# Kernel optimization log

Hardware: AMD Instinct MI355X
Metric: run time of the kernel (lower is better)

The kernel has to match this reference:

```python
import jax, jax.numpy as jnp
import numpy as np

N_NODES = 100000
N_EDGES = 1600000
IN_DIM = 128
EM_DIM = 64
HI_DIM = 64
OUT_DIM = 128
HEADS = 4


def setup_inputs() -> dict:
    key = jax.random.key(0)
    ks = jax.random.split(key, 16)
    s = 0.05  # small init scale to keep exp(a) well-conditioned
    return {
        "x_from": jax.random.normal(ks[0], (N_NODES, IN_DIM), jnp.float32),
        "edge_index": jax.random.randint(ks[1], (2, N_EDGES), 0, N_NODES, jnp.int32),
        "Wi1": jax.random.normal(ks[2], (HEADS, IN_DIM, EM_DIM), jnp.float32) * s,
        "bi1": jax.random.normal(ks[3], (HEADS, EM_DIM), jnp.float32) * s,
        "Wi2": jax.random.normal(ks[4], (HEADS, EM_DIM, EM_DIM), jnp.float32) * s,
        "bi2": jax.random.normal(ks[5], (HEADS, EM_DIM), jnp.float32) * s,
        "Wa1": jax.random.normal(ks[6], (HEADS, 2 * EM_DIM, HI_DIM), jnp.float32) * s,
        "ba1": jax.random.normal(ks[7], (HEADS, HI_DIM), jnp.float32) * s,
        "Wa2": jax.random.normal(ks[8], (HEADS, HI_DIM, 1), jnp.float32) * s,
        "ba2": jax.random.normal(ks[9], (HEADS, 1), jnp.float32) * s,
        "Wf1": jax.random.normal(ks[10], (HEADS * EM_DIM, HI_DIM), jnp.float32) * s,
        "bf1": jax.random.normal(ks[11], (HI_DIM,), jnp.float32) * s,
        "Wf2": jax.random.normal(ks[12], (HI_DIM, OUT_DIM), jnp.float32) * s,
        "bf2": jax.random.normal(ks[13], (OUT_DIM,), jnp.float32) * s,
    }


def reference(x_from, edge_index, Wi1, bi1, Wi2, bi2, Wa1, ba1, Wa2, ba2,
              Wf1, bf1, Wf2, bf2):
    n = x_from.shape[0]
    src, dst = edge_index[0], edge_index[1]

    # per-head node embedding MLP (layer_n=2, leaky_relu between layers)
    h1 = jax.nn.leaky_relu(jnp.einsum('nf,hfe->hne', x_from, Wi1) + bi1[:, None, :])
    hs = jnp.einsum('hne,hed->hnd', h1, Wi2) + bi2[:, None, :]  # [H, N, EM]
    # hs_to in the original is f_init(x_from) again -> identical to hs

    em = hs.shape[-1]
    # A(cat(h_src, h_dst)) first linear split per-node to avoid [H,E,2*EM] cat
    s_src = jnp.einsum('hne,hek->hnk', hs, Wa1[:, :em, :])  # [H, N, HI]
    s_dst = jnp.einsum('hne,hek->hnk', hs, Wa1[:, em:, :])  # [H, N, HI]
    t = jax.nn.leaky_relu(s_src[:, src] + s_dst[:, dst] + ba1[:, None, :])  # [H, E, HI]
    a = jax.nn.leaky_relu(jnp.einsum('hek,hko->heo', t, Wa2) + ba2[:, None, :])  # [H,E,1]

    e = jnp.exp(a)  # [H, E, 1]
    # softmax denominator is scatter_add over SRC (as in the source)
    e_sum = jax.vmap(lambda v: jax.ops.segment_sum(v, src, num_segments=n))(e)  # [H,N,1]
    alpha = e / e_sum[:, src]  # [H, E, 1]

    # attention-weighted aggregation: scatter_add of hs[src]*alpha onto dst
    msg = hs[:, src] * alpha  # [H, E, EM]
    agg = jax.vmap(lambda v: jax.ops.segment_sum(v, dst, num_segments=n))(msg)  # [H,N,EM]

    h_cat = jnp.transpose(agg, (1, 0, 2)).reshape(n, -1)  # [N, H*EM], head-major cat
    out = jax.nn.leaky_relu(h_cat @ Wf1 + bf1) @ Wf2 + bf2  # [N, OUT]
    return out
```

## Files before the change

kernel.cpp:

```cpp
#include <hip/hip_runtime.h>
#include <hip/hip_fp16.h>

#define NN 100000
#define NE 1600000
#define HEADS 4
#define EM 64
#define HF 256
#define IN_DIM 128
#define HI 64
#define OUT_DIM 128
#define NB_SCAN 391
#define SLOTS 56

using f16 = _Float16;
typedef _Float16 f16x2 __attribute__((ext_vector_type(2)));
typedef _Float16 f16x4 __attribute__((ext_vector_type(4)));
typedef float f32x2 __attribute__((ext_vector_type(2)));
typedef float f32x4 __attribute__((ext_vector_type(4)));
typedef int i32x4 __attribute__((ext_vector_type(4)));

__device__ __forceinline__ float lrelu(float x) { return fmaxf(x, 0.01f * x); }

__global__ __launch_bounds__(256) void k_wprep(
    const float* __restrict__ Wi1, const float* __restrict__ Wi2, const float* __restrict__ Wa1,
    uint2* __restrict__ Wi1f, uint2* __restrict__ Wi2f,
    uint2* __restrict__ Wsf, uint2* __restrict__ Wdf)
{
    int tid = blockIdx.x * 256 + threadIdx.x;
    int chunk = tid >> 6, lane = tid & 63;
    if (chunk >= 320) return;
    int g = lane >> 4, c = lane & 15;
    const float* wp;
    uint2* dst;
    if (chunk < 128) {
        int h = chunk >> 5, kc = (chunk >> 2) & 7, n = chunk & 3;
        wp = Wi1 + (size_t)h * IN_DIM * EM + (size_t)(kc * 16 + 4 * g) * EM + n * 16 + c;
        dst = Wi1f + chunk * 64 + lane;
    } else if (chunk < 192) {
        int idx = chunk - 128;
        int h = idx >> 4, kc = (idx >> 2) & 3, n = idx & 3;
        wp = Wi2 + (size_t)h * EM * EM + (size_t)(kc * 16 + 4 * g) * EM + n * 16 + c;
        dst = Wi2f + idx * 64 + lane;
    } else if (chunk < 256) {
        int idx = chunk - 192;
        int h = idx >> 4, kc = (idx >> 2) & 3, n = idx & 3;
        wp = Wa1 + (size_t)h * (2 * EM) * HI + (size_t)(kc * 16 + 4 * g) * HI + n * 16 + c;
        dst = Wsf + idx * 64 + lane;
    } else {
        int idx = chunk - 256;
        int h = idx >> 4, kc = (idx >> 2) & 3, n = idx & 3;
        wp = Wa1 + (size_t)h * (2 * EM) * HI + (size_t)(EM + kc * 16 + 4 * g) * HI + n * 16 + c;
        dst = Wdf + idx * 64 + lane;
    }
    f16x4 v = { (f16)wp[0], (f16)wp[EM], (f16)wp[2 * EM], (f16)wp[3 * EM] };
    *dst = __builtin_bit_cast(uint2, v);
}

__global__ __launch_bounds__(256) void k_embed(
    const float* __restrict__ x,
    const float* __restrict__ bi1, const float* __restrict__ bi2,
    const uint2* __restrict__ Wi1f, const uint2* __restrict__ Wi2f,
    const uint2* __restrict__ Wsf, const uint2* __restrict__ Wdf,
    const int* __restrict__ ei, int* __restrict__ cur_s, int* __restrict__ cur_d,
    int* __restrict__ es1,
    f16* __restrict__ hs, f16* __restrict__ ssrc, f16* __restrict__ sdst)
{
    __shared__ __align__(16) char smem[18432];
    f16 (*xh)[136]     = (f16(*)[136])smem;
    f16 (*hsL)[16][72] = (f16(*)[16][72])smem;
    f16 (*h1L)[16][72] = (f16(*)[16][72])(smem + 9216);

    const int t = threadIdx.x;
    const int base = blockIdx.x * 16;

    #pragma unroll
    for (int i = 0; i < 2; ++i) {
        int q = t + i * 256;
        int row = q >> 5;
        int c4 = (q & 31) << 2;
        float4 v = *(const float4*)(x + (size_t)(base + row) * IN_DIM + c4);
        f16x4 hv = { (f16)v.x, (f16)v.y, (f16)v.z, (f16)v.w };
        *(f16x4*)&xh[row][c4] = hv;
    }
    __syncthreads();

    const int h = t >> 6;
    const int l = t & 63;
    const int g = l >> 4;
    const int c = l & 15;

    const f32x4 z4 = { 0.f, 0.f, 0.f, 0.f };

    f32x4 acc1[4] = { z4, z4, z4, z4 };
    {
        const uint2* Wf = Wi1f + (size_t)h * 32 * 64;
        for (int kc = 0; kc < 8; ++kc) {
            f16x4 bf[4];
            #pragma unroll
            for (int n = 0; n < 4; ++n)
                bf[n] = __builtin_bit_cast(f16x4, Wf[(kc * 4 + n) * 64 + l]);
            f16x4 af = *(const f16x4*)&xh[c][kc * 16 + 4 * g];
            #pragma unroll
            for (int n = 0; n < 4; ++n)
                acc1[n] = __builtin_amdgcn_mfma_f32_16x16x16f16(af, bf[n], acc1[n], 0, 0, 0);
        }
    }
    __syncthreads();

    #pragma unroll
    for (int n = 0; n < 4; ++n) {
        float b = bi1[h * EM + n * 16 + c];
        #pragma unroll
        for (int r = 0; r < 4; ++r)
            h1L[h][4 * g + r][n * 16 + c] = (f16)lrelu(acc1[n][r] + b);
    }
    __syncthreads();

    f32x4 acc2[4] = { z4, z4, z4, z4 };
    {
        const uint2* Wf = Wi2f + (size_t)h * 16 * 64;
        for (int kc = 0; kc < 4; ++kc) {
            f16x4 bf[4];
            #pragma unroll
            for (int n = 0; n < 4; ++n)
                bf[n] = __builtin_bit_cast(f16x4, Wf[(kc * 4 + n) * 64 + l]);
            f16x4 af = *(const f16x4*)&h1L[h][c][kc * 16 + 4 * g];
            #pragma unroll
            for (int n = 0; n < 4; ++n)
                acc2[n] = __builtin_amdgcn_mfma_f32_16x16x16f16(af, bf[n], acc2[n], 0, 0, 0);
        }
    }
    #pragma unroll
    for (int n = 0; n < 4; ++n) {
        float b = bi2[h * EM + n * 16 + c];
        #pragma unroll
        for (int r = 0; r < 4; ++r)
            hsL[h][4 * g + r][n * 16 + c] = (f16)(acc2[n][r] + b);
    }
    __syncthreads();

    f16x4 af3[4];
    #pragma unroll
    for (int kc = 0; kc < 4; ++kc)
        af3[kc] = *(const f16x4*)&hsL[h][c][kc * 16 + 4 * g];

    {
        f32x4 acc3[4] = { z4, z4, z4, z4 };
        const uint2* Wf = Wsf + (size_t)h * 16 * 64;
        for (int kc = 0; kc < 4; ++kc) {
            f16x4 bf[4];
            #pragma unroll
            for (int n = 0; n < 4; ++n)
                bf[n] = __builtin_bit_cast(f16x4, Wf[(kc * 4 + n) * 64 + l]);
            #pragma unroll
            for (int n = 0; n < 4; ++n)
                acc3[n] = __builtin_amdgcn_mfma_f32_16x16x16f16(af3[kc], bf[n], acc3[n], 0, 0, 0);
        }
        #pragma unroll
        for (int n = 0; n < 4; ++n)
            #pragma unroll
            for (int r = 0; r < 4; ++r)
                h1L[h][4 * g + r][n * 16 + c] = (f16)acc3[n][r];
    }
    f32x4 acc3b[4] = { z4, z4, z4, z4 };
    {
        const uint2* Wf = Wdf + (size_t)h * 16 * 64;
        for (int kc = 0; kc < 4; ++kc) {
            f16x4 bf[4];
            #pragma unroll
            for (int n = 0; n < 4; ++n)
                bf[n] = __builtin_bit_cast(f16x4, Wf[(kc * 4 + n) * 64 + l]);
            #pragma unroll
            for (int n = 0; n < 4; ++n)
                acc3b[n] = __builtin_amdgcn_mfma_f32_16x16x16f16(af3[kc], bf[n], acc3b[n], 0, 0, 0);
        }
    }
    __syncthreads();

    #pragma unroll
    for (int i = 0; i < 2; ++i) {
        int q = t + i * 256;
        int hd = q >> 7, row = (q >> 3) & 15, c8 = (q & 7) << 3;
        int node = base + row;
        *(int4*)&hs[(size_t)node * HF + hd * EM + c8]   = *(int4*)&hsL[hd][row][c8];
        *(int4*)&ssrc[(size_t)node * HF + hd * EM + c8] = *(int4*)&h1L[hd][row][c8];
    }
    __syncthreads();

    #pragma unroll
    for (int n = 0; n < 4; ++n)
        #pragma unroll
        for (int r = 0; r < 4; ++r)
            hsL[h][4 * g + r][n * 16 + c] = (f16)acc3b[n][r];
    __syncthreads();
    #pragma unroll
    for (int i = 0; i < 2; ++i) {
        int q = t + i * 256;
        int hd = q >> 7, row = (q >> 3) & 15, c8 = (q & 7) << 3;
        int node = base + row;
        *(int4*)&sdst[(size_t)node * HF + hd * EM + c8] = *(int4*)&hsL[hd][row][c8];
    }

    {
        int e = blockIdx.x * 256 + t;
        int src = ei[e], dst = ei[NE + e];
        int pos_d = atomicAdd(cur_d + dst, 1);
        int pos_s = atomicAdd(cur_s + src, 1);
        if (pos_s < SLOTS) es1[src * SLOTS + pos_s] = (pos_d << 17) | dst;
    }
}

__global__ __launch_bounds__(256) void k_scan1(const int* __restrict__ arr, int* __restrict__ bsum)
{
    const int t = threadIdx.x, lane = t & 63, w = t >> 6;
    int i = blockIdx.x * 256 + t;
    int v = (i < NN) ? arr[i] : 0;
    #pragma unroll
    for (int d = 1; d < 64; d <<= 1) v += __shfl_xor(v, d);
    __shared__ int ws[4];
    if (lane == 0) ws[w] = v;
    __syncthreads();
    if (t == 0) bsum[blockIdx.x] = ws[0] + ws[1] + ws[2] + ws[3];
}

__global__ __launch_bounds__(256) void k_scan2(int* __restrict__ bsum)
{
    __shared__ int wsum[4], woff[4];
    __shared__ int base, ctot;
    const int t = threadIdx.x, lane = t & 63, w = t >> 6;
    if (t == 0) base = 0;
    __syncthreads();
    for (int start = 0; start < NB_SCAN; start += 256) {
        int i = start + t;
        int v = (i < NB_SCAN) ? bsum[i] : 0;
        int incl = v;
        #pragma unroll
        for (int d = 1; d < 64; d <<= 1) {
            int u = __shfl_up(incl, d);
            if (lane >= d) incl += u;
        }
        if (lane == 63) wsum[w] = incl;
        __syncthreads();
        if (t == 0) {
            int s = 0;
            #pragma unroll
            for (int j = 0; j < 4; ++j) { int xv = wsum[j]; woff[j] = s; s += xv; }
            ctot = s;
        }
        __syncthreads();
        if (i < NB_SCAN) bsum[i] = base + woff[w] + incl - v;
        __syncthreads();
        if (t == 0) base += ctot;
        __syncthreads();
    }
}

__global__ __launch_bounds__(256) void k_scan3(int* __restrict__ arr, const int* __restrict__ bsum)
{
    const int t = threadIdx.x, lane = t & 63, w = t >> 6;
    int i = blockIdx.x * 256 + t;
    int v = (i < NN) ? arr[i] : 0;
    int incl = v;
    #pragma unroll
    for (int d = 1; d < 64; d <<= 1) {
        int u = __shfl_up(incl, d);
        if (lane >= d) incl += u;
    }
    __shared__ int wsum[4], woff[4];
    if (lane == 63) wsum[w] = incl;
    __syncthreads();
    if (t == 0) {
        int s = 0;
        #pragma unroll
        for (int j = 0; j < 4; ++j) { int xv = wsum[j]; woff[j] = s; s += xv; }
    }
    __syncthreads();
    if (i < NN) arr[i] = bsum[blockIdx.x] + woff[w] + incl - v;
}

__global__ __launch_bounds__(256) void k_edge_att_csr(
    const int* __restrict__ es1, const int* __restrict__ cur_s,
    const f16* __restrict__ ssrc, const f16* __restrict__ sdst,
    const float* __restrict__ ba1, const float* __restrict__ Wa2, const float* __restrict__ ba2,
    const int* __restrict__ cur_d, i32x4* __restrict__ ed16, float* __restrict__ inv4)
{
    const int wave = threadIdx.x >> 6;
    const int lane = threadIdx.x & 63;
    const int n = blockIdx.x * 4 + wave;
    const int eidx = lane >> 4;
    const int q = lane & 15;
    const int h = q >> 2;
    const int fb = q * 16;

    int cnt = cur_s[n];
    if (cnt <= 0) return;
    if (cnt > SLOTS) cnt = SLOTS;

    int bslot = lane < cnt ? lane : cnt - 1;
    const int bval = es1[n * SLOTS + bslot];
    const int bdst = bval & 0x1FFFF;
    const int brec = cur_d[bdst] + (bval >> 17);

    f16x2 z[8], w[8];
    {
        const int4* sr = (const int4*)(ssrc + (size_t)n * HF + fb);
        int4 s0 = sr[0], s1 = sr[1];
        const f16x2* sp0 = (const f16x2*)&s0;
        const f16x2* sp1 = (const f16x2*)&s1;
        const float4* bb = (const float4*)(ba1 + fb);
        const float4* wwp = (const float4*)(Wa2 + fb);
        #pragma unroll
        for (int j = 0; j < 4; ++j) {
            float4 b4 = bb[j];
            float4 w4 = wwp[j];
            f16x2 blo = { (f16)b4.x, (f16)b4.y }, bhi = { (f16)b4.z, (f16)b4.w };
            f16x2 wlo = { (f16)w4.x, (f16)w4.y }, whi = { (f16)w4.z, (f16)w4.w };
            f16x2 sv = (j < 2) ? sp0[2 * j] : sp1[2 * (j - 2)];
            f16x2 sv2 = (j < 2) ? sp0[2 * j + 1] : sp1[2 * (j - 2) + 1];
            z[2 * j] = sv + blo;
            z[2 * j + 1] = sv2 + bhi;
            w[2 * j] = wlo;
            w[2 * j + 1] = whi;
        }
    }
    const float ba2v = ba2[h];
    const f16x2 c001 = { (f16)0.01f, (f16)0.01f };

    float esumv = 0.f;

    int r = 0;
    int slot0 = r + eidx; if (slot0 > cnt - 1) slot0 = cnt - 1;
    bool val = (r + eidx) < cnt;
    int dst_cur = __shfl(bdst, slot0);
    int rec_cur = __shfl(brec, slot0);
    const int4* dr = (const int4*)(sdst + (size_t)dst_cur * HF + fb);
    int4 d0 = dr[0], d1 = dr[1];

    while (r < cnt) {
        const int rn = r + 4;
        int4 nd0 = d0, nd1 = d1;
        int dst_nxt = dst_cur, rec_nxt = rec_cur;
        bool val_n = false;
        if (rn < cnt) {
            int slot = rn + eidx; if (slot > cnt - 1) slot = cnt - 1;
            val_n = (rn + eidx) < cnt;
            dst_nxt = __shfl(bdst, slot);
            rec_nxt = __shfl(brec, slot);
            const int4* dr2 = (const int4*)(sdst + (size_t)dst_nxt * HF + fb);
            nd0 = dr2[0]; nd1 = dr2[1];
        }

        const f16x2* dp0 = (const f16x2*)&d0;
        const f16x2* dp1 = (const f16x2*)&d1;
        float s = 0.f;
        #pragma unroll
        for (int j = 0; j < 4; ++j) {
            f16x2 u = z[j] + dp0[j];
            u = __builtin_elementwise_max(u, u * c001);
            s = __builtin_amdgcn_fdot2(u, w[j], s, false);
        }
        #pragma unroll
        for (int j = 0; j < 4; ++j) {
            f16x2 u = z[4 + j] + dp1[j];
            u = __builtin_elementwise_max(u, u * c001);
            s = __builtin_amdgcn_fdot2(u, w[4 + j], s, false);
        }
        s += __shfl_xor(s, 1);
        s += __shfl_xor(s, 2);
        float a = s + ba2v;
        a = fmaxf(a, 0.01f * a);
        float eh = val ? __expf(a) : 0.f;
        esumv += eh;

        {
            int b = lane & 48;
            float e1 = __shfl(eh, b + 4);
            float e2 = __shfl(eh, b + 8);
            float e3 = __shfl(eh, b + 12);
            if (val && q == 0) {
                f16x2 p01 = { (f16)eh, (f16)e1 };
                f16x2 p23 = { (f16)e2, (f16)e3 };
                i32x4 rec;
                rec.x = n;
                rec.y = 0;
                rec.z = (int)__builtin_bit_cast(uint, p01);
                rec.w = (int)__builtin_bit_cast(uint, p23);
                __builtin_nontemporal_store(rec, &ed16[rec_cur]);
            }
        }

        d0 = nd0; d1 = nd1; dst_cur = dst_nxt; rec_cur = rec_nxt; val = val_n;
        r = rn;
    }

    esumv += __shfl_xor(esumv, 16);
    esumv += __shfl_xor(esumv, 32);

    if (eidx == 0 && (q & 3) == 0)
        inv4[n * 4 + h] = 1.f / esumv;
}

__global__ __launch_bounds__(256) void k_aggregate_csr(
    const i32x4* __restrict__ ed16, const int* __restrict__ cur_d,
    const float* __restrict__ inv4,
    const f16* __restrict__ hs,
    f16* __restrict__ agg)
{
    const int wave = threadIdx.x >> 6;
    const int lane = threadIdx.x & 63;
    const int n = blockIdx.x * 4 + wave;
    const int eidx = lane >> 4;
    const int q = lane & 15;
    const int h = q >> 2;
    const int fb = q * 16;

    const int beg = cur_d[n];
    const int end = (n < NN - 1) ? cur_d[n + 1] : NE;

    const f32x2 z2 = { 0.f, 0.f };
    f32x2 acc[8];
    #pragma unroll
    for (int j = 0; j < 8; ++j) acc[j] = z2;

#define COMP_B(recV, ivV, hV0, hV1, valV)                                       \
    {                                                                           \
        uint sel = (h & 2) ? (uint)recV.w : (uint)recV.z;                       \
        f16x2 selh = __builtin_bit_cast(f16x2, sel);                            \
        float att = (float)((h & 1) ? selh.y : selh.x);                         \
        float al = valV ? att * ivV : 0.f;                                      \
        f32x2 al2 = { al, al };                                                 \
        const f16x2* hp0 = (const f16x2*)&hV0;                                  \
        const f16x2* hp1 = (const f16x2*)&hV1;                                  \
        _Pragma("unroll")                                                       \
        for (int j = 0; j < 4; ++j) {                                           \
            f16x2 f = hp0[j];                                                   \
            f32x2 fv = { (float)f.x, (float)f.y };                              \
            acc[j] += fv * al2;                                                 \
        }                                                                       \
        _Pragma("unroll")                                                       \
        for (int j = 0; j < 4; ++j) {                                           \
            f16x2 f = hp1[j];                                                   \
            f32x2 fv = { (float)f.x, (float)f.y };                              \
            acc[4 + j] += fv * al2;                                             \
        }                                                                       \
    }

    if (beg < end) {
        int p = beg;
        int idx0 = p + eidx; if (idx0 > end - 1) idx0 = end - 1;
        bool val = (p + eidx) < end;
        i32x4 rec = __builtin_nontemporal_load(&ed16[idx0]);
        float iv = inv4[rec.x * 4 + h];
        const int4* hr = (const int4*)(hs + (size_t)rec.x * HF + fb);
        int4 v0 = hr[0], v1 = hr[1];

        while (p < end) {
            const int pn = p + 4;
            i32x4 nrec = rec;
            float niv = iv;
            int4 nv0 = v0, nv1 = v1;
            bool val_n = false;
            if (pn < end) {
                int idx = pn + eidx; if (idx > end - 1) idx = end - 1;
                val_n = (pn + eidx) < end;
                nrec = __builtin_nontemporal_load(&ed16[idx]);
                niv = inv4[nrec.x * 4 + h];
                const int4* hr2 = (const int4*)(hs + (size_t)nrec.x * HF + fb);
                nv0 = hr2[0]; nv1 = hr2[1];
            }

            COMP_B(rec, iv, v0, v1, val);

            rec = nrec; iv = niv; v0 = nv0; v1 = nv1; val = val_n;
            p = pn;
        }
    }
#undef COMP_B

    #pragma unroll
    for (int j = 0; j < 8; ++j) {
        acc[j].x += __shfl_xor(acc[j].x, 16);
        acc[j].x += __shfl_xor(acc[j].x, 32);
        acc[j].y += __shfl_xor(acc[j].y, 16);
        acc[j].y += __shfl_xor(acc[j].y, 32);
    }

    if (eidx == 0) {
        int4 o0, o1;
        f16x2* op0 = (f16x2*)&o0;
        f16x2* op1 = (f16x2*)&o1;
        #pragma unroll
        for (int j = 0; j < 4; ++j) {
            op0[j] = (f16x2){ (f16)acc[j].x, (f16)acc[j].y };
            op1[j] = (f16x2){ (f16)acc[4 + j].x, (f16)acc[4 + j].y };
        }
        int4* ar = (int4*)(agg + (size_t)n * HF + fb);
        ar[0] = o0; ar[1] = o1;
    }
}

__global__ __launch_bounds__(256) void k_out_mlp2(
    const f16* __restrict__ agg,
    const float* __restrict__ Wf1, const float* __restrict__ bf1,
    const float* __restrict__ Wf2, const float* __restrict__ bf2,
    float* __restrict__ out)
{
    __shared__ __align__(16) f16 aggL[64][272];
    __shared__ __align__(16) f16 midL[64][72];

    const int t = threadIdx.x;
    const int base = blockIdx.x * 64;

    #pragma unroll
    for (int i = 0; i < 8; ++i) {
        int q = t + i * 256;
        int row = q >> 5, c8 = (q & 31) << 3;
        int gr = base + row; if (gr >= NN) gr = NN - 1;
        *(int4*)&aggL[row][c8] = *(const int4*)&agg[(size_t)gr * HF + c8];
    }
    __syncthreads();

    const int w = t >> 6, l = t & 63;
    const int g = l >> 4, c = l & 15;
    const f32x4 z4 = { 0.f, 0.f, 0.f, 0.f };

    {
        f32x4 acc[4] = { z4, z4, z4, z4 };
        for (int kc = 0; kc < 16; ++kc) {
            const float* wp = Wf1 + (size_t)(kc * 16 + 4 * g) * HI + w * 16 + c;
            f16x4 bf;
            bf[0] = (f16)wp[0]; bf[1] = (f16)wp[HI]; bf[2] = (f16)wp[2 * HI]; bf[3] = (f16)wp[3 * HI];
            #pragma unroll
            for (int m = 0; m < 4; ++m) {
                f16x4 af = *(const f16x4*)&aggL[m * 16 + c][kc * 16 + 4 * g];
                acc[m] = __builtin_amdgcn_mfma_f32_16x16x16f16(af, bf, acc[m], 0, 0, 0);
            }
        }
        float b = bf1[w * 16 + c];
        #pragma unroll
        for (int m = 0; m < 4; ++m)
            #pragma unroll
            for (int r = 0; r < 4; ++r)
                midL[m * 16 + 4 * g + r][w * 16 + c] = (f16)lrelu(acc[m][r] + b);
    }
    __syncthreads();

    #pragma unroll
    for (int nb = 0; nb < 2; ++nb) {
        int nt = w + nb * 4;
        f32x4 acc[4] = { z4, z4, z4, z4 };
        for (int kc = 0; kc < 4; ++kc) {
            const float* wp = Wf2 + (size_t)(kc * 16 + 4 * g) * OUT_DIM + nt * 16 + c;
            f16x4 bf;
            bf[0] = (f16)wp[0]; bf[1] = (f16)wp[OUT_DIM]; bf[2] = (f16)wp[2 * OUT_DIM]; bf[3] = (f16)wp[3 * OUT_DIM];
            #pragma unroll
            for (int m = 0; m < 4; ++m) {
                f16x4 af = *(const f16x4*)&midL[m * 16 + c][kc * 16 + 4 * g];
                acc[m] = __builtin_amdgcn_mfma_f32_16x16x16f16(af, bf, acc[m], 0, 0, 0);
            }
        }
        float b = bf2[nt * 16 + c];
        #pragma unroll
        for (int m = 0; m < 4; ++m)
            #pragma unroll
            for (int r = 0; r < 4; ++r) {
                int node = base + m * 16 + 4 * g + r;
                if (node < NN) out[(size_t)node * OUT_DIM + nt * 16 + c] = acc[m][r] + b;
            }
    }
}

extern "C" void kernel_launch(void* const* d_in, const int* in_sizes, int n_in,
                              void* d_out, int out_size, void* d_ws, size_t ws_size,
                              hipStream_t stream) {
    const float* x   = (const float*)d_in[0];
    const int*   ei  = (const int*)d_in[1];
    const float* Wi1 = (const float*)d_in[2];
    const float* bi1 = (const float*)d_in[3];
    const float* Wi2 = (const float*)d_in[4];
    const float* bi2 = (const float*)d_in[5];
    const float* Wa1 = (const float*)d_in[6];
    const float* ba1 = (const float*)d_in[7];
    const float* Wa2 = (const float*)d_in[8];
    const float* ba2 = (const float*)d_in[9];
    const float* Wf1 = (const float*)d_in[10];
    const float* bf1 = (const float*)d_in[11];
    const float* Wf2 = (const float*)d_in[12];
    const float* bf2 = (const float*)d_in[13];
    float* out = (float*)d_out;

    const size_t HS_B     = (size_t)NN * HF * sizeof(f16);
    const size_t OFF_SSRC = HS_B;
    const size_t OFF_SDST = 2 * HS_B;
    const size_t OFF_ES1  = 3 * HS_B;
    const size_t OFF_INV  = OFF_ES1 + (size_t)NN * SLOTS * sizeof(int);
    const size_t OFF_CURS = OFF_INV + (size_t)NN * 4 * sizeof(float);
    const size_t OFF_CURD = OFF_CURS + (size_t)NN * sizeof(int);
    const size_t OFF_BSUM = OFF_CURD + (size_t)NN * sizeof(int);
    const size_t OFF_WF   = (OFF_BSUM + NB_SCAN * sizeof(int) + 15) & ~(size_t)15;
    const size_t WI1F_B = 4 * 8 * 4 * 64 * 8;
    const size_t WI2F_B = 4 * 4 * 4 * 64 * 8;
    const size_t NEED   = OFF_WF + WI1F_B + 3 * WI2F_B;
    if (ws_size < NEED) return;

    char* ws = (char*)d_ws;
    f16*   hs   = (f16*)(ws);
    f16*   ssrc = (f16*)(ws + OFF_SSRC);
    f16*   sdst = (f16*)(ws + OFF_SDST);
    int*   es1  = (int*)(ws + OFF_ES1);
    float* inv4 = (float*)(ws + OFF_INV);
    int*   cur_s = (int*)(ws + OFF_CURS);
    int*   cur_d = (int*)(ws + OFF_CURD);
    int*   bsum  = (int*)(ws + OFF_BSUM);
    uint2* Wi1f = (uint2*)(ws + OFF_WF);
    uint2* Wi2f = (uint2*)(ws + OFF_WF + WI1F_B);
    uint2* Wsf  = (uint2*)(ws + OFF_WF + WI1F_B + WI2F_B);
    uint2* Wdf  = (uint2*)(ws + OFF_WF + WI1F_B + 2 * WI2F_B);
    f16*   agg  = (f16*)(ws + OFF_SSRC);
    i32x4* ed16 = (i32x4*)d_out;

    const int NB16 = NN / 16;
    const int NB64 = (NN + 63) / 64;

    (void)hipMemsetAsync(cur_s, 0, 2 * (size_t)NN * sizeof(int), stream);
    k_wprep<<<80, 256, 0, stream>>>(Wi1, Wi2, Wa1, Wi1f, Wi2f, Wsf, Wdf);
    k_embed<<<NB16, 256, 0, stream>>>(x, bi1, bi2, Wi1f, Wi2f, Wsf, Wdf,
                                      ei, cur_s, cur_d, es1, hs, ssrc, sdst);

    k_scan1<<<NB_SCAN, 256, 0, stream>>>(cur_d, bsum);
    k_scan2<<<1, 256, 0, stream>>>(bsum);
    k_scan3<<<NB_SCAN, 256, 0, stream>>>(cur_d, bsum);

    k_edge_att_csr<<<NN / 4, 256, 0, stream>>>(es1, cur_s, ssrc, sdst, ba1, Wa2, ba2,
                                               cur_d, ed16, inv4);

    k_aggregate_csr<<<NN / 4, 256, 0, stream>>>(ed16, cur_d, inv4, hs, agg);

    k_out_mlp2<<<NB64, 256, 0, stream>>>(agg, Wf1, bf1, Wf2, bf2, out);
}
```

Measured before the change: 512.8 us.

## Fold Wi2 into attention weights to compute hs, s_src, s_dst in parallel

A new small kernel precomputes Wi2·Wa1 products and bias terms bi2·Wa1 per head, so the s_src and s_dst projections are taken directly from h1 instead of from hs. In the embed kernel the three 64x64 MFMA chains now run in one loop from the same A fragments. This removes a shared-memory round trip and a barrier, and shortens the dependent MFMA chain. It adds a tiny serial weight-combination kernel, and the folded weights are rounded to fp16 once instead of rounding the intermediate hs.

```diff
diff --git a/kernel.cpp b/kernel.cpp
--- a/kernel.cpp
+++ b/kernel.cpp
@@ -22,13 +22,12 @@
 __device__ __forceinline__ float lrelu(float x) { return fmaxf(x, 0.01f * x); }
 
 __global__ __launch_bounds__(256) void k_wprep(
-    const float* __restrict__ Wi1, const float* __restrict__ Wi2, const float* __restrict__ Wa1,
-    uint2* __restrict__ Wi1f, uint2* __restrict__ Wi2f,
-    uint2* __restrict__ Wsf, uint2* __restrict__ Wdf)
+    const float* __restrict__ Wi1, const float* __restrict__ Wi2,
+    uint2* __restrict__ Wi1f, uint2* __restrict__ Wi2f)
 {
     int tid = blockIdx.x * 256 + threadIdx.x;
     int chunk = tid >> 6, lane = tid & 63;
-    if (chunk >= 320) return;
+    if (chunk >= 192) return;
     int g = lane >> 4, c = lane & 15;
     const float* wp;
     uint2* dst;
@@ -36,24 +35,49 @@
         int h = chunk >> 5, kc = (chunk >> 2) & 7, n = chunk & 3;
         wp = Wi1 + (size_t)h * IN_DIM * EM + (size_t)(kc * 16 + 4 * g) * EM + n * 16 + c;
         dst = Wi1f + chunk * 64 + lane;
-    } else if (chunk < 192) {
+    } else {
         int idx = chunk - 128;
         int h = idx >> 4, kc = (idx >> 2) & 3, n = idx & 3;
         wp = Wi2 + (size_t)h * EM * EM + (size_t)(kc * 16 + 4 * g) * EM + n * 16 + c;
         dst = Wi2f + idx * 64 + lane;
-    } else if (chunk < 256) {
-        int idx = chunk - 192;
-        int h = idx >> 4, kc = (idx >> 2) & 3, n = idx & 3;
-        wp = Wa1 + (size_t)h * (2 * EM) * HI + (size_t)(kc * 16 + 4 * g) * HI + n * 16 + c;
-        dst = Wsf + idx * 64 + lane;
-    } else {
-        int idx = chunk - 256;
-        int h = idx >> 4, kc = (idx >> 2) & 3, n = idx & 3;
-        wp = Wa1 + (size_t)h * (2 * EM) * HI + (size_t)(EM + kc * 16 + 4 * g) * HI + n * 16 + c;
-        dst = Wdf + idx * 64 + lane;
     }
     f16x4 v = { (f16)wp[0], (f16)wp[EM], (f16)wp[2 * EM], (f16)wp[3 * EM] };
     *dst = __builtin_bit_cast(uint2, v);
+}
+
+__global__ __launch_bounds__(256) void k_wcomb(
+    const float* __restrict__ Wi2, const float* __restrict__ Wa1, const float* __restrict__ bi2,
+    uint2* __restrict__ Wsf, uint2* __restrict__ Wdf,
+    float* __restrict__ bcs, float* __restrict__ bcd)
+{
+    const int h = blockIdx.x >> 1, m = blockIdx.x & 1;
+    const float* W2 = Wi2 + (size_t)h * EM * EM;
+    const float* Wa = Wa1 + (size_t)h * (2 * EM) * HI + (m ? EM * HI : 0);
+    uint2* outw = (m ? Wdf : Wsf) + h * 16 * 64;
+    float* bc   = (m ? bcd : bcs) + h * 64;
+    const int t = threadIdx.x;
+
+    for (int e = t; e < 1024; e += 256) {
+        int chunk = e >> 6, lane = e & 63;
+        int g = (lane >> 4), c = lane & 15;
+        int kc = chunk >> 2, n = chunk & 3;
+        int col = n * 16 + c;
+        int f0 = kc * 16 + 4 * g;
+        f16x4 v;
+        #pragma unroll
+        for (int j = 0; j < 4; ++j) {
+            float s = 0.f;
+            for (int k = 0; k < EM; ++k)
+                s += W2[(f0 + j) * EM + k] * Wa[k * HI + col];
+            v[j] = (f16)s;
+        }
+        outw[chunk * 64 + lane] = __builtin_bit_cast(uint2, v);
+    }
+    if (t < 64) {
+        float s = 0.f;
+        for (int k = 0; k < EM; ++k) s += bi2[h * EM + k] * Wa[k * HI + t];
+        bc[t] = s;
+    }
 }
 
 __global__ __launch_bounds__(256) void k_embed(
@@ -61,6 +85,7 @@
     const float* __restrict__ bi1, const float* __restrict__ bi2,
     const uint2* __restrict__ Wi1f, const uint2* __restrict__ Wi2f,
     const uint2* __restrict__ Wsf, const uint2* __restrict__ Wdf,
+    const float* __restrict__ bcs, const float* __restrict__ bcd,
     const int* __restrict__ ei, int* __restrict__ cur_s, int* __restrict__ cur_d,
     int* __restrict__ es1,
     f16* __restrict__ hs, f16* __restrict__ ssrc, f16* __restrict__ sdst)
@@ -116,63 +141,39 @@
     }
     __syncthreads();
 
-    f32x4 acc2[4] = { z4, z4, z4, z4 };
-    {
-        const uint2* Wf = Wi2f + (size_t)h * 16 * 64;
-        for (int kc = 0; kc < 4; ++kc) {
-            f16x4 bf[4];
-            #pragma unroll
-            for (int n = 0; n < 4; ++n)
-                bf[n] = __builtin_bit_cast(f16x4, Wf[(kc * 4 + n) * 64 + l]);
-            f16x4 af = *(const f16x4*)&h1L[h][c][kc * 16 + 4 * g];
-            #pragma unroll
-            for (int n = 0; n < 4; ++n)
-                acc2[n] = __builtin_amdgcn_mfma_f32_16x16x16f16(af, bf[n], acc2[n], 0, 0, 0);
-        }
-    }
-    #pragma unroll
-    for (int n = 0; n < 4; ++n) {
-        float b = bi2[h * EM + n * 16 + c];
-        #pragma unroll
-        for (int r = 0; r < 4; ++r)
-            hsL[h][4 * g + r][n * 16 + c] = (f16)(acc2[n][r] + b);
-    }
-    __syncthreads();
-
     f16x4 af3[4];
     #pragma unroll
     for (int kc = 0; kc < 4; ++kc)
-        af3[kc] = *(const f16x4*)&hsL[h][c][kc * 16 + 4 * g];
-
-    {
-        f32x4 acc3[4] = { z4, z4, z4, z4 };
-        const uint2* Wf = Wsf + (size_t)h * 16 * 64;
-        for (int kc = 0; kc < 4; ++kc) {
-            f16x4 bf[4];
-            #pragma unroll
-            for (int n = 0; n < 4; ++n)
-                bf[n] = __builtin_bit_cast(f16x4, Wf[(kc * 4 + n) * 64 + l]);
-            #pragma unroll
-            for (int n = 0; n < 4; ++n)
-                acc3[n] = __builtin_amdgcn_mfma_f32_16x16x16f16(af3[kc], bf[n], acc3[n], 0, 0, 0);
-        }
-        #pragma unroll
-        for (int n = 0; n < 4; ++n)
-            #pragma unroll
-            for (int r = 0; r < 4; ++r)
-                h1L[h][4 * g + r][n * 16 + c] = (f16)acc3[n][r];
-    }
+        af3[kc] = *(const f16x4*)&h1L[h][c][kc * 16 + 4 * g];
+
+    f32x4 acc2[4]  = { z4, z4, z4, z4 };
+    f32x4 acc3[4]  = { z4, z4, z4, z4 };
     f32x4 acc3b[4] = { z4, z4, z4, z4 };
     {
-        const uint2* Wf = Wdf + (size_t)h * 16 * 64;
+        const uint2* W2 = Wi2f + (size_t)h * 16 * 64;
+        const uint2* Ws = Wsf  + (size_t)h * 16 * 64;
+        const uint2* Wd = Wdf  + (size_t)h * 16 * 64;
         for (int kc = 0; kc < 4; ++kc) {
-            f16x4 bf[4];
-            #pragma unroll
-            for (int n = 0; n < 4; ++n)
-                bf[n] = __builtin_bit_cast(f16x4, Wf[(kc * 4 + n) * 64 + l]);
-            #pragma unroll
-            for (int n = 0; n < 4; ++n)
-                acc3b[n] = __builtin_amdgcn_mfma_f32_16x16x16f16(af3[kc], bf[n], acc3b[n], 0, 0, 0);
+            #pragma unroll
+            for (int n = 0; n < 4; ++n) {
+                f16x4 b2 = __builtin_bit_cast(f16x4, W2[(kc * 4 + n) * 64 + l]);
+                f16x4 bs = __builtin_bit_cast(f16x4, Ws[(kc * 4 + n) * 64 + l]);
+                f16x4 bd = __builtin_bit_cast(f16x4, Wd[(kc * 4 + n) * 64 + l]);
+                acc2[n]  = __builtin_amdgcn_mfma_f32_16x16x16f16(af3[kc], b2, acc2[n], 0, 0, 0);
+                acc3[n]  = __builtin_amdgcn_mfma_f32_16x16x16f16(af3[kc], bs, acc3[n], 0, 0, 0);
+                acc3b[n] = __builtin_amdgcn_mfma_f32_16x16x16f16(af3[kc], bd, acc3b[n], 0, 0, 0);
+            }
+        }
+    }
+
+    #pragma unroll
+    for (int n = 0; n < 4; ++n) {
+        float b2 = bi2[h * EM + n * 16 + c];
+        float b3 = bcs[h * EM + n * 16 + c];
+        #pragma unroll
+        for (int r = 0; r < 4; ++r) {
+            hsL[h][4 * g + r][n * 16 + c] = (f16)(acc2[n][r] + b2);
+            h1L[h][4 * g + r][n * 16 + c] = (f16)(acc3[n][r] + b3);
         }
     }
     __syncthreads();
@@ -188,10 +189,12 @@
     __syncthreads();
 
     #pragma unroll
-    for (int n = 0; n < 4; ++n)
+    for (int n = 0; n < 4; ++n) {
+        float b = bcd[h * EM + n * 16 + c];
         #pragma unroll
         for (int r = 0; r < 4; ++r)
-            hsL[h][4 * g + r][n * 16 + c] = (f16)acc3b[n][r];
+            hsL[h][4 * g + r][n * 16 + c] = (f16)(acc3b[n][r] + b);
+    }
     __syncthreads();
     #pragma unroll
     for (int i = 0; i < 2; ++i) {
@@ -600,7 +603,8 @@
     const size_t OFF_WF   = (OFF_BSUM + NB_SCAN * sizeof(int) + 15) & ~(size_t)15;
     const size_t WI1F_B = 4 * 8 * 4 * 64 * 8;
     const size_t WI2F_B = 4 * 4 * 4 * 64 * 8;
-    const size_t NEED   = OFF_WF + WI1F_B + 3 * WI2F_B;
+    const size_t OFF_BC = OFF_WF + WI1F_B + 3 * WI2F_B;
+    const size_t NEED   = OFF_BC + 2 * 256 * sizeof(float);
     if (ws_size < NEED) return;
 
     char* ws = (char*)d_ws;
@@ -616,6 +620,8 @@
     uint2* Wi2f = (uint2*)(ws + OFF_WF + WI1F_B);
     uint2* Wsf  = (uint2*)(ws + OFF_WF + WI1F_B + WI2F_B);
     uint2* Wdf  = (uint2*)(ws + OFF_WF + WI1F_B + 2 * WI2F_B);
+    float* bcs  = (float*)(ws + OFF_BC);
+    float* bcd  = (float*)(ws + OFF_BC + 256 * sizeof(float));
     f16*   agg  = (f16*)(ws + OFF_SSRC);
     i32x4* ed16 = (i32x4*)d_out;
 
@@ -623,8 +629,9 @@
     const int NB64 = (NN + 63) / 64;
 
     (void)hipMemsetAsync(cur_s, 0, 2 * (size_t)NN * sizeof(int), stream);
-    k_wprep<<<80, 256, 0, stream>>>(Wi1, Wi2, Wa1, Wi1f, Wi2f, Wsf, Wdf);
-    k_embed<<<NB16, 256, 0, stream>>>(x, bi1, bi2, Wi1f, Wi2f, Wsf, Wdf,
+    k_wprep<<<48, 256, 0, stream>>>(Wi1, Wi2, Wi1f, Wi2f);
+    k_wcomb<<<8, 256, 0, stream>>>(Wi2, Wa1, bi2, Wsf, Wdf, bcs, bcd);
+    k_embed<<<NB16, 256, 0, stream>>>(x, bi1, bi2, Wi1f, Wi2f, Wsf, Wdf, bcs, bcd,
                                       ei, cur_s, cur_d, es1, hs, ssrc, sdst);
 
     k_scan1<<<NB_SCAN, 256, 0, stream>>>(cur_d, bsum);
```

Measured after the change: 538.8 us. +5.1%, slower.
